# Kernel optimization log

Measured on AMD Instinct MI355X. Metric: run time of the kernel, lower is better.

## Reference

```python
import jax, jax.numpy as jnp
import numpy as np

B, CIN, COUT, H, W, K, KH, KW = 32, 256, 256, 56, 56, 4, 3, 3
STRIDE, PAD = (1, 1), [(1, 1), (1, 1)]


def setup_inputs() -> dict:
    key = jax.random.key(0)
    ks = jax.random.split(key, 8)
    s_w = 1.0 / np.sqrt(CIN * KH * KW)
    return {
        "x": jax.random.normal(ks[0], (B, CIN, H, W), jnp.float32),
        "weight": jax.random.normal(ks[1], (K, COUT, CIN, KH, KW), jnp.float32) * s_w,
        "bias": jax.random.normal(ks[2], (K, COUT), jnp.float32) * s_w,
        "fc1_w": jax.random.normal(ks[3], (K, CIN), jnp.float32) / np.sqrt(CIN),
        "fc1_b": jax.random.normal(ks[4], (K,), jnp.float32) * 0.01,
        "fc2_w": jax.random.normal(ks[5], (K, K), jnp.float32) / np.sqrt(K),
        "fc2_b": jax.random.normal(ks[6], (K,), jnp.float32) * 0.01,
    }


def reference(x, weight, bias, fc1_w, fc1_b, fc2_w, fc2_b):
    # Attention2D: global avg pool -> 1x1 conv (dense) -> relu -> 1x1 conv -> softmax
    pooled = x.mean(axis=(2, 3))                                  # [B, CIN]
    a = jax.nn.relu(jnp.einsum('bc,kc->bk', pooled, fc1_w) + fc1_b)
    att = jax.nn.softmax(jnp.einsum('bk,jk->bj', a, fc2_w) + fc2_b, axis=1)  # [B, K]

    # Aggregate per-sample weights/bias over K experts
    agg_w = jnp.einsum('bk,koihw->boihw', att, weight)            # [B, COUT, CIN, KH, KW]
    agg_b = att @ bias                                            # [B, COUT]

    # Per-sample conv == grouped conv with groups=B in the torch original
    def conv_one(xi, wi):
        return jax.lax.conv_general_dilated(
            xi[None], wi, window_strides=STRIDE, padding=PAD,
            dimension_numbers=('NCHW', 'OIHW', 'NCHW'))[0]

    out = jax.vmap(conv_one)(x, agg_w)                            # [B, COUT, H, W]
    return out + agg_b[:, :, None, None]
```

## Files before the change

kernel.cpp:

```cpp
#include <hip/hip_runtime.h>
#include <hip/hip_bf16.h>
#include <stdint.h>

#define BB   32
#define CIN  256
#define COUT 256
#define HH   56
#define WW   56
#define HW   3136
#define KEXP 4

typedef __attribute__((ext_vector_type(8))) short  short8;
typedef __attribute__((ext_vector_type(4))) float  floatx4;

__device__ __forceinline__ unsigned short f2bf(float f) {
    uint32_t u = __float_as_uint(f);
    u = (u + 0x7fffu + ((u >> 16) & 1u)) >> 16;
    return (unsigned short)u;
}
__device__ __forceinline__ float bf2f(unsigned short s) {
    return __uint_as_float(((uint32_t)s) << 16);
}
__device__ __forceinline__ uint32_t pack2(float a, float b) {
    return (uint32_t)f2bf(a) | ((uint32_t)f2bf(b) << 16);
}

__device__ __forceinline__ void async_copy16(const void* gsrc, void* ldst) {
    __builtin_amdgcn_global_load_lds(
        (const __attribute__((address_space(1))) unsigned int*)gsrc,
        (__attribute__((address_space(3))) unsigned int*)ldst, 16, 0, 0);
}

__global__ __launch_bounds__(256) void transpose_pool_kernel(
    const float* __restrict__ x,
    unsigned short* __restrict__ xt,
    float* __restrict__ pooled)
{
    __shared__ unsigned short tile[CIN * 62];
    const int bx  = blockIdx.x;
    const int b   = bx / HH;
    const int h   = bx % HH;
    const int tid = threadIdx.x;

    const float* xb = x + (size_t)b * CIN * HW + h * WW;

    for (int i = tid; i < CIN * 14; i += 256) {
        const int c  = i / 14;
        const int wv = i % 14;
        const float4 v = *(const float4*)(xb + (size_t)c * HW + wv * 4);
        uint32_t* p = (uint32_t*)&tile[c * 62 + wv * 4];
        p[0] = pack2(v.x, v.y);
        p[1] = pack2(v.z, v.w);
    }
    __syncthreads();

    {
        const int c = tid;
        float s = 0.f;
        #pragma unroll 8
        for (int i = 0; i < WW; ++i) s += bf2f(tile[c * 62 + i]);
        atomicAdd(&pooled[b * CIN + c], s * (1.0f / (float)HW));
    }

    for (int j = tid; j < WW * CIN; j += 256) {
        const int w = j >> 8;
        const int c = j & 255;
        xt[(((size_t)b * HH + h) * WW + w) * CIN + c] = tile[c * 62 + w];
    }
}

__global__ __launch_bounds__(64) void attn_kernel(
    const float* __restrict__ pooled,
    const float* __restrict__ fc1w,
    const float* __restrict__ fc1b,
    const float* __restrict__ fc2w,
    const float* __restrict__ fc2b,
    float* __restrict__ att)
{
    const int b    = blockIdx.x;
    const int lane = threadIdx.x;
    const float* pb = pooled + b * CIN;

    float s[KEXP] = {0.f, 0.f, 0.f, 0.f};
    #pragma unroll
    for (int c0 = 0; c0 < CIN; c0 += 64) {
        const float p = pb[c0 + lane];
        #pragma unroll
        for (int k = 0; k < KEXP; ++k) s[k] += p * fc1w[k * CIN + c0 + lane];
    }
    #pragma unroll
    for (int off = 32; off > 0; off >>= 1) {
        #pragma unroll
        for (int k = 0; k < KEXP; ++k) s[k] += __shfl_down(s[k], off);
    }
    if (lane == 0) {
        float a[KEXP];
        #pragma unroll
        for (int k = 0; k < KEXP; ++k) a[k] = fmaxf(s[k] + fc1b[k], 0.f);
        float z[KEXP], m = -1e30f;
        #pragma unroll
        for (int j = 0; j < KEXP; ++j) {
            float t = fc2b[j];
            #pragma unroll
            for (int k = 0; k < KEXP; ++k) t += a[k] * fc2w[j * KEXP + k];
            z[j] = t;
            m = fmaxf(m, t);
        }
        float den = 0.f;
        #pragma unroll
        for (int j = 0; j < KEXP; ++j) { z[j] = expf(z[j] - m); den += z[j]; }
        const float inv = 1.0f / den;
        #pragma unroll
        for (int j = 0; j < KEXP; ++j) att[b * KEXP + j] = z[j] * inv;
    }
}

__global__ __launch_bounds__(256) void aggw_kernel(
    const float* __restrict__ weight,
    const float* __restrict__ bias,
    const float* __restrict__ att,
    unsigned short* __restrict__ aggw,
    float* __restrict__ aggb)
{
    __shared__ float accw[CIN * 9];
    const int bx  = blockIdx.x;
    const int b   = bx >> 8;
    const int o   = bx & 255;
    const int tid = threadIdx.x;

    float av[KEXP];
    #pragma unroll
    for (int k = 0; k < KEXP; ++k) av[k] = att[b * KEXP + k];

    float r[9];
    #pragma unroll
    for (int j = 0; j < 9; ++j) r[j] = 0.f;
    #pragma unroll
    for (int k = 0; k < KEXP; ++k) {
        const float* wk = weight + (size_t)(k * COUT + o) * (CIN * 9);
        #pragma unroll
        for (int j = 0; j < 9; ++j) r[j] += av[k] * wk[j * 256 + tid];
    }
    #pragma unroll
    for (int j = 0; j < 9; ++j) accw[j * 256 + tid] = r[j];
    __syncthreads();

    #pragma unroll
    for (int j = 0; j < 9; ++j) {
        const float v = accw[tid * 9 + j];
        aggw[(((size_t)b * 9 + j) * COUT + o) * CIN + tid] = f2bf(v);
    }
    if (tid == 0) {
        float s = 0.f;
        #pragma unroll
        for (int k = 0; k < KEXP; ++k) s += av[k] * bias[k * COUT + o];
        aggb[b * COUT + o] = s;
    }
}

__global__ __launch_bounds__(256) void conv_gemm_kernel(
    const unsigned short* __restrict__ xt,
    const unsigned short* __restrict__ aggw,
    const float* __restrict__ aggb,
    const unsigned short* __restrict__ zbuf,
    float* __restrict__ out)
{
    __shared__ unsigned short As[128 * 64];
    __shared__ unsigned short Bs[128 * 64];

    const int bx   = blockIdx.x;
    const int slot = bx >> 3;
    const int xcd  = bx & 7;
    const int b    = xcd + 8 * (slot / 50);
    const int rr   = slot % 50;
    const int pt   = rr >> 1;
    const int ot   = rr & 1;
    const int o0   = ot * 128;
    const int p0   = pt * 128;

    const int tid  = threadIdx.x;
    const int wave = tid >> 6;
    const int lane = tid & 63;
    const int lrow = lane >> 3;
    const int lxor = ((lane & 7) ^ lrow) * 16;

    const char* aggw_b = (const char*)aggw + (size_t)b * 9 * COUT * CIN * 2;
    const char* xt_b   = (const char*)xt   + (size_t)b * HW * CIN * 2;
    const char* zb     = (const char*)zbuf;

    int aoff[4];
    int boff[4], bh[4], bw[4], bval[4];
    #pragma unroll
    for (int j = 0; j < 4; ++j) {
        const int rowl = j * 32 + wave * 8 + lrow;
        aoff[j] = (o0 + rowl) * 512 + lxor;
        const int p = p0 + rowl;
        bh[j]   = p / 56;
        bw[j]   = p % 56;
        bval[j] = (p < HW);
        boff[j] = p * 512 + lxor;
    }

    floatx4 acc[4][4];
    #pragma unroll
    for (int mi = 0; mi < 4; ++mi)
        #pragma unroll
        for (int ni = 0; ni < 4; ++ni)
            #pragma unroll
            for (int i = 0; i < 4; ++i) acc[mi][ni][i] = 0.f;

    const int row_base = (wave >> 1) * 64;
    const int col_base = (wave & 1) * 64;
    const int m_off    = lane & 15;
    const int q        = lane >> 4;
    const int sx       = m_off & 7;

    for (int kt = 0; kt < 36; ++kt) {
        const int rs = kt >> 2;
        const int c0 = (kt & 3) * 64;
        const int dh = rs / 3 - 1;
        const int dw = rs % 3 - 1;

        const int a_kt = rs * (COUT * CIN * 2) + c0 * 2;
        const int b_kt = (dh * 56 + dw) * 512 + c0 * 2;

        #pragma unroll
        for (int j = 0; j < 4; ++j) {
            async_copy16(aggw_b + (size_t)(aoff[j] + a_kt),
                         &As[(j * 32 + wave * 8) * 64]);
        }
        #pragma unroll
        for (int j = 0; j < 4; ++j) {
            const int h2 = bh[j] + dh;
            const int w2 = bw[j] + dw;
            const bool ok = bval[j] && ((unsigned)h2 < 56u) && ((unsigned)w2 < 56u);
            const char* src = ok ? (xt_b + (size_t)(boff[j] + b_kt))
                                 : (zb + lxor);
            async_copy16(src, &Bs[(j * 32 + wave * 8) * 64]);
        }
        __syncthreads();

        #pragma unroll
        for (int ks = 0; ks < 2; ++ks) {
            short8 af[4], bf[4];
            #pragma unroll
            for (int mi = 0; mi < 4; ++mi)
                af[mi] = *(const short8*)((const char*)As
                          + (row_base + mi * 16 + m_off) * 128
                          + (((ks * 4 + q) ^ sx) * 16));
            #pragma unroll
            for (int ni = 0; ni < 4; ++ni)
                bf[ni] = *(const short8*)((const char*)Bs
                          + (col_base + ni * 16 + m_off) * 128
                          + (((ks * 4 + q) ^ sx) * 16));
            #pragma unroll
            for (int mi = 0; mi < 4; ++mi)
                #pragma unroll
                for (int ni = 0; ni < 4; ++ni)
                    acc[mi][ni] = __builtin_amdgcn_mfma_f32_16x16x32_bf16(
                        af[mi], bf[ni], acc[mi][ni], 0, 0, 0);
        }
        __syncthreads();
    }

    float* outb = out + (size_t)b * COUT * HW;
    const int g4 = (lane >> 4) * 4;
    #pragma unroll
    for (int mi = 0; mi < 4; ++mi) {
        #pragma unroll
        for (int i = 0; i < 4; ++i) {
            const int o = o0 + row_base + mi * 16 + g4 + i;
            const float bv = aggb[b * COUT + o];
            #pragma unroll
            for (int ni = 0; ni < 4; ++ni) {
                const int p = p0 + col_base + ni * 16 + m_off;
                if (p < HW) outb[(size_t)o * HW + p] = acc[mi][ni][i] + bv;
            }
        }
    }
}

extern "C" void kernel_launch(void* const* d_in, const int* in_sizes, int n_in,
                              void* d_out, int out_size, void* d_ws, size_t ws_size,
                              hipStream_t stream) {
    const float* x      = (const float*)d_in[0];
    const float* weight = (const float*)d_in[1];
    const float* bias   = (const float*)d_in[2];
    const float* fc1w   = (const float*)d_in[3];
    const float* fc1b   = (const float*)d_in[4];
    const float* fc2w   = (const float*)d_in[5];
    const float* fc2b   = (const float*)d_in[6];
    float* out = (float*)d_out;

    char* ws = (char*)d_ws;
    unsigned short* xt     = (unsigned short*)(ws);
    unsigned short* aggw   = (unsigned short*)(ws + 51380224);
    float*          pooled = (float*)(ws + 89128960);
    float*          att    = (float*)(ws + 89161728);
    float*          aggb   = (float*)(ws + 89162240);
    unsigned short* zbuf   = (unsigned short*)(ws + 89195008);

    hipMemsetAsync((void*)pooled, 0, 32768, stream);
    hipMemsetAsync((void*)zbuf,   0, 256,   stream);

    transpose_pool_kernel<<<BB * HH, 256, 0, stream>>>(x, xt, pooled);
    attn_kernel<<<BB, 64, 0, stream>>>(pooled, fc1w, fc1b, fc2w, fc2b, att);
    aggw_kernel<<<BB * COUT, 256, 0, stream>>>(weight, bias, att, aggw, aggb);
    conv_gemm_kernel<<<BB * 2 * 25, 256, 0, stream>>>(xt, aggw, aggb, zbuf, out);
}
```

Measured before the change: 403.2 us.

## Pad transposed input with zero halo and batch weight aggregation per output

Result: faster. 367.6 us (-8.8%).

```diff
diff --git a/kernel.cpp b/kernel.cpp
--- a/kernel.cpp
+++ b/kernel.cpp
@@ -9,6 +9,7 @@
 #define WW   56
 #define HW   3136
 #define KEXP 4
+#define HP   58
 
 typedef __attribute__((ext_vector_type(8))) short  short8;
 typedef __attribute__((ext_vector_type(4))) float  floatx4;
@@ -34,7 +35,7 @@
 __global__ __launch_bounds__(256) void transpose_pool_kernel(
     const float* __restrict__ x,
     unsigned short* __restrict__ xt,
-    float* __restrict__ pooled)
+    float* __restrict__ partial)
 {
     __shared__ unsigned short tile[CIN * 62];
     const int bx  = blockIdx.x;
@@ -55,63 +56,85 @@
     __syncthreads();
 
     {
-        const int c = tid;
         float s = 0.f;
         #pragma unroll 8
-        for (int i = 0; i < WW; ++i) s += bf2f(tile[c * 62 + i]);
-        atomicAdd(&pooled[b * CIN + c], s * (1.0f / (float)HW));
-    }
-
-    for (int j = tid; j < WW * CIN; j += 256) {
-        const int w = j >> 8;
-        const int c = j & 255;
-        xt[(((size_t)b * HH + h) * WW + w) * CIN + c] = tile[c * 62 + w];
-    }
-}
-
-__global__ __launch_bounds__(64) void attn_kernel(
-    const float* __restrict__ pooled,
+        for (int i = 0; i < WW; ++i) s += bf2f(tile[tid * 62 + i]);
+        partial[((size_t)b * HH + h) * CIN + tid] = s;
+    }
+
+    unsigned short* row = xt + (((size_t)b * HP + (h + 1)) * HP) * CIN;
+    for (int j = tid; j < WW * 128; j += 256) {
+        const int w  = j >> 7;
+        const int c2 = (j & 127) * 2;
+        const uint32_t v = (uint32_t)tile[c2 * 62 + w]
+                         | ((uint32_t)tile[(c2 + 1) * 62 + w] << 16);
+        *(uint32_t*)&row[(w + 1) * CIN + c2] = v;
+    }
+
+    if (tid < 128) {
+        ((uint32_t*)&row[0])[tid]          = 0u;
+        ((uint32_t*)&row[57 * CIN])[tid]   = 0u;
+    }
+    if (h == 0) {
+        uint32_t* r0  = (uint32_t*)(xt + ((size_t)b * HP + 0)  * HP * CIN);
+        uint32_t* r57 = (uint32_t*)(xt + ((size_t)b * HP + 57) * HP * CIN);
+        for (int i = tid; i < HP * 128; i += 256) { r0[i] = 0u; r57[i] = 0u; }
+    }
+}
+
+__global__ __launch_bounds__(256) void attn_kernel(
+    const float* __restrict__ partial,
     const float* __restrict__ fc1w,
     const float* __restrict__ fc1b,
     const float* __restrict__ fc2w,
     const float* __restrict__ fc2b,
     float* __restrict__ att)
 {
-    const int b    = blockIdx.x;
-    const int lane = threadIdx.x;
-    const float* pb = pooled + b * CIN;
-
-    float s[KEXP] = {0.f, 0.f, 0.f, 0.f};
-    #pragma unroll
-    for (int c0 = 0; c0 < CIN; c0 += 64) {
-        const float p = pb[c0 + lane];
-        #pragma unroll
-        for (int k = 0; k < KEXP; ++k) s[k] += p * fc1w[k * CIN + c0 + lane];
-    }
-    #pragma unroll
-    for (int off = 32; off > 0; off >>= 1) {
-        #pragma unroll
-        for (int k = 0; k < KEXP; ++k) s[k] += __shfl_down(s[k], off);
-    }
-    if (lane == 0) {
-        float a[KEXP];
-        #pragma unroll
-        for (int k = 0; k < KEXP; ++k) a[k] = fmaxf(s[k] + fc1b[k], 0.f);
-        float z[KEXP], m = -1e30f;
-        #pragma unroll
-        for (int j = 0; j < KEXP; ++j) {
-            float t = fc2b[j];
-            #pragma unroll
-            for (int k = 0; k < KEXP; ++k) t += a[k] * fc2w[j * KEXP + k];
-            z[j] = t;
-            m = fmaxf(m, t);
-        }
-        float den = 0.f;
-        #pragma unroll
-        for (int j = 0; j < KEXP; ++j) { z[j] = expf(z[j] - m); den += z[j]; }
-        const float inv = 1.0f / den;
-        #pragma unroll
-        for (int j = 0; j < KEXP; ++j) att[b * KEXP + j] = z[j] * inv;
+    __shared__ float pl[CIN];
+    const int b   = blockIdx.x;
+    const int tid = threadIdx.x;
+
+    float s = 0.f;
+    const float* pp = partial + (size_t)b * HH * CIN + tid;
+    #pragma unroll 8
+    for (int h = 0; h < HH; ++h) s += pp[h * CIN];
+    pl[tid] = s * (1.0f / (float)HW);
+    __syncthreads();
+
+    if (tid < 64) {
+        const int lane = tid;
+        float sk[KEXP] = {0.f, 0.f, 0.f, 0.f};
+        #pragma unroll
+        for (int c0 = 0; c0 < CIN; c0 += 64) {
+            const float p = pl[c0 + lane];
+            #pragma unroll
+            for (int k = 0; k < KEXP; ++k) sk[k] += p * fc1w[k * CIN + c0 + lane];
+        }
+        #pragma unroll
+        for (int off = 32; off > 0; off >>= 1) {
+            #pragma unroll
+            for (int k = 0; k < KEXP; ++k) sk[k] += __shfl_down(sk[k], off);
+        }
+        if (lane == 0) {
+            float a[KEXP];
+            #pragma unroll
+            for (int k = 0; k < KEXP; ++k) a[k] = fmaxf(sk[k] + fc1b[k], 0.f);
+            float z[KEXP], m = -1e30f;
+            #pragma unroll
+            for (int j = 0; j < KEXP; ++j) {
+                float t = fc2b[j];
+                #pragma unroll
+                for (int k = 0; k < KEXP; ++k) t += a[k] * fc2w[j * KEXP + k];
+                z[j] = t;
+                m = fmaxf(m, t);
+            }
+            float den = 0.f;
+            #pragma unroll
+            for (int j = 0; j < KEXP; ++j) { z[j] = expf(z[j] - m); den += z[j]; }
+            const float inv = 1.0f / den;
+            #pragma unroll
+            for (int j = 0; j < KEXP; ++j) att[b * KEXP + j] = z[j] * inv;
+        }
     }
 }
 
@@ -124,37 +147,49 @@
 {
     __shared__ float accw[CIN * 9];
     const int bx  = blockIdx.x;
-    const int b   = bx >> 8;
-    const int o   = bx & 255;
+    const int o   = bx >> 2;
+    const int b0  = (bx & 3) * 8;
     const int tid = threadIdx.x;
 
-    float av[KEXP];
-    #pragma unroll
-    for (int k = 0; k < KEXP; ++k) av[k] = att[b * KEXP + k];
-
-    float r[9];
-    #pragma unroll
-    for (int j = 0; j < 9; ++j) r[j] = 0.f;
+    float wreg[KEXP][9];
     #pragma unroll
     for (int k = 0; k < KEXP; ++k) {
         const float* wk = weight + (size_t)(k * COUT + o) * (CIN * 9);
         #pragma unroll
-        for (int j = 0; j < 9; ++j) r[j] += av[k] * wk[j * 256 + tid];
-    }
-    #pragma unroll
-    for (int j = 0; j < 9; ++j) accw[j * 256 + tid] = r[j];
-    __syncthreads();
-
-    #pragma unroll
-    for (int j = 0; j < 9; ++j) {
-        const float v = accw[tid * 9 + j];
-        aggw[(((size_t)b * 9 + j) * COUT + o) * CIN + tid] = f2bf(v);
-    }
-    if (tid == 0) {
-        float s = 0.f;
-        #pragma unroll
-        for (int k = 0; k < KEXP; ++k) s += av[k] * bias[k * COUT + o];
-        aggb[b * COUT + o] = s;
+        for (int j = 0; j < 9; ++j) wreg[k][j] = wk[j * 256 + tid];
+    }
+    float bvals[KEXP];
+    #pragma unroll
+    for (int k = 0; k < KEXP; ++k) bvals[k] = bias[k * COUT + o];
+
+    for (int bi = 0; bi < 8; ++bi) {
+        const int b = b0 + bi;
+        float av[KEXP];
+        #pragma unroll
+        for (int k = 0; k < KEXP; ++k) av[k] = att[b * KEXP + k];
+
+        __syncthreads();
+        #pragma unroll
+        for (int j = 0; j < 9; ++j) {
+            float r = 0.f;
+            #pragma unroll
+            for (int k = 0; k < KEXP; ++k) r += av[k] * wreg[k][j];
+            accw[j * 256 + tid] = r;
+        }
+        __syncthreads();
+
+        for (int i = tid; i < 9 * 128; i += 256) {
+            const int j  = i >> 7;
+            const int cp = (i & 127) * 2;
+            const uint32_t v = pack2(accw[cp * 9 + j], accw[(cp + 1) * 9 + j]);
+            *(uint32_t*)&aggw[(((size_t)b * 9 + j) * COUT + o) * CIN + cp] = v;
+        }
+        if (tid == 0) {
+            float sb = 0.f;
+            #pragma unroll
+            for (int k = 0; k < KEXP; ++k) sb += av[k] * bvals[k];
+            aggb[b * COUT + o] = sb;
+        }
     }
 }
 
@@ -162,7 +197,6 @@
     const unsigned short* __restrict__ xt,
     const unsigned short* __restrict__ aggw,
     const float* __restrict__ aggb,
-    const unsigned short* __restrict__ zbuf,
     float* __restrict__ out)
 {
     __shared__ unsigned short As[128 * 64];
@@ -185,20 +219,18 @@
     const int lxor = ((lane & 7) ^ lrow) * 16;
 
     const char* aggw_b = (const char*)aggw + (size_t)b * 9 * COUT * CIN * 2;
-    const char* xt_b   = (const char*)xt   + (size_t)b * HW * CIN * 2;
-    const char* zb     = (const char*)zbuf;
-
-    int aoff[4];
-    int boff[4], bh[4], bw[4], bval[4];
+    const char* xt_b   = (const char*)xt   + (size_t)b * HP * HP * CIN * 2;
+
+    int aoff[4], boff[4];
     #pragma unroll
     for (int j = 0; j < 4; ++j) {
         const int rowl = j * 32 + wave * 8 + lrow;
         aoff[j] = (o0 + rowl) * 512 + lxor;
-        const int p = p0 + rowl;
-        bh[j]   = p / 56;
-        bw[j]   = p % 56;
-        bval[j] = (p < HW);
-        boff[j] = p * 512 + lxor;
+        const int p  = p0 + rowl;
+        const int pv = (p < HW) ? p : 0;
+        const int h  = pv / 56;
+        const int w  = pv % 56;
+        boff[j] = ((h + 1) * HP + (w + 1)) * 512 + lxor;
     }
 
     floatx4 acc[4][4];
@@ -222,22 +254,16 @@
         const int dw = rs % 3 - 1;
 
         const int a_kt = rs * (COUT * CIN * 2) + c0 * 2;
-        const int b_kt = (dh * 56 + dw) * 512 + c0 * 2;
-
-        #pragma unroll
-        for (int j = 0; j < 4; ++j) {
+        const int b_kt = (dh * HP + dw) * 512 + c0 * 2;
+
+        #pragma unroll
+        for (int j = 0; j < 4; ++j)
             async_copy16(aggw_b + (size_t)(aoff[j] + a_kt),
                          &As[(j * 32 + wave * 8) * 64]);
-        }
-        #pragma unroll
-        for (int j = 0; j < 4; ++j) {
-            const int h2 = bh[j] + dh;
-            const int w2 = bw[j] + dw;
-            const bool ok = bval[j] && ((unsigned)h2 < 56u) && ((unsigned)w2 < 56u);
-            const char* src = ok ? (xt_b + (size_t)(boff[j] + b_kt))
-                                 : (zb + lxor);
-            async_copy16(src, &Bs[(j * 32 + wave * 8) * 64]);
-        }
+        #pragma unroll
+        for (int j = 0; j < 4; ++j)
+            async_copy16(xt_b + (size_t)(boff[j] + b_kt),
+                         &Bs[(j * 32 + wave * 8) * 64]);
         __syncthreads();
 
         #pragma unroll
@@ -293,18 +319,14 @@
     float* out = (float*)d_out;
 
     char* ws = (char*)d_ws;
-    unsigned short* xt     = (unsigned short*)(ws);
-    unsigned short* aggw   = (unsigned short*)(ws + 51380224);
-    float*          pooled = (float*)(ws + 89128960);
-    float*          att    = (float*)(ws + 89161728);
-    float*          aggb   = (float*)(ws + 89162240);
-    unsigned short* zbuf   = (unsigned short*)(ws + 89195008);
-
-    hipMemsetAsync((void*)pooled, 0, 32768, stream);
-    hipMemsetAsync((void*)zbuf,   0, 256,   stream);
-
-    transpose_pool_kernel<<<BB * HH, 256, 0, stream>>>(x, xt, pooled);
-    attn_kernel<<<BB, 64, 0, stream>>>(pooled, fc1w, fc1b, fc2w, fc2b, att);
-    aggw_kernel<<<BB * COUT, 256, 0, stream>>>(weight, bias, att, aggw, aggb);
-    conv_gemm_kernel<<<BB * 2 * 25, 256, 0, stream>>>(xt, aggw, aggb, zbuf, out);
-}
+    unsigned short* xt      = (unsigned short*)(ws);
+    unsigned short* aggw    = (unsigned short*)(ws + 55115776);
+    float*          partial = (float*)(ws + 92864512);
+    float*          att     = (float*)(ws + 94699520);
+    float*          aggb    = (float*)(ws + 94700032);
+
+    transpose_pool_kernel<<<BB * HH, 256, 0, stream>>>(x, xt, partial);
+    attn_kernel<<<BB, 256, 0, stream>>>(partial, fc1w, fc1b, fc2w, fc2b, att);
+    aggw_kernel<<<COUT * 4, 256, 0, stream>>>(weight, bias, att, aggw, aggb);
+    conv_gemm_kernel<<<BB * 2 * 25, 256, 0, stream>>>(xt, aggw, aggb, out);
+}
```
